# Kernel tuning notes

Measured on AMD Instinct MI355X. Metric: run time of the kernel, lower is better.

## Reference

```python
import jax, jax.numpy as jnp
import numpy as np

NUM_EXPERTS = 16
TOP_K = 2
D_IN = 1024
D_HID = 4096
D_OUT = 1024
BATCH = 8192


def setup_inputs() -> dict:
    key = jax.random.key(0)
    ks = jax.random.split(key, 6)
    s_in = 1.0 / np.sqrt(D_IN)
    s_hid = 1.0 / np.sqrt(D_HID)
    return {
        "x": jax.random.normal(ks[0], (BATCH, D_IN), dtype=jnp.float32),
        "Wg": jax.random.normal(ks[1], (D_IN, NUM_EXPERTS), dtype=jnp.float32) * s_in,
        "W1": jax.random.normal(ks[2], (NUM_EXPERTS, D_IN, D_HID), dtype=jnp.float32) * s_in,
        "b1": jnp.zeros((NUM_EXPERTS, D_HID), dtype=jnp.float32),
        "W2": jax.random.normal(ks[3], (NUM_EXPERTS, D_HID, D_OUT), dtype=jnp.float32) * s_hid,
        "b2": jnp.zeros((NUM_EXPERTS, D_OUT), dtype=jnp.float32),
    }


def _moe_forward(x, Wg, W1, b1, W2, b2):
    # Gating: top-k routing with softmax over the selected logits.
    logits = x @ Wg                                   # [B, E]
    top_vals, top_idx = jax.lax.top_k(logits, TOP_K)  # [B, k]
    routing_weights = jax.nn.softmax(top_vals, axis=-1)  # [B, k]

    # Per-token combine weight for each expert (sum over k slots):
    # cw[b, e] = sum_k routing_weights[b, k] * (top_idx[b, k] == e)
    one_hot = jax.nn.one_hot(top_idx, NUM_EXPERTS, dtype=x.dtype)  # [B, k, E]
    combine_w = jnp.einsum("bk,bke->be", routing_weights, one_hot)  # [B, E]

    # Per-expert MLP compute + weighted scatter-add combine.
    # Fixed-size loop over experts (structurally distinct weight slices);
    # equivalent math to the original's gather/compute/scatter dispatch.
    out = jnp.zeros((x.shape[0], D_OUT), dtype=x.dtype)
    for e in range(NUM_EXPERTS):
        h = jax.nn.relu(x @ W1[e] + b1[e])            # [B, H]
        y = h @ W2[e] + b2[e]                         # [B, O]
        out = out + combine_w[:, e:e + 1] * y
    return out


def reference(x, Wg, W1, b1, W2, b2):
    return _moe_forward(x, Wg, W1, b1, W2, b2)
```

## Files before the change

kernel.cpp:

```cpp
#include <hip/hip_runtime.h>
#include <cstdio>

#define DIN   1024
#define DHID  4096
#define DOUT  1024
#define NEXP  16
#define NTOK  8192
#define NPAIR (NTOK * 2)
#define PADMAX 18432
#define MAXTILES 144

typedef _Float16 h8 __attribute__((ext_vector_type(8)));
typedef _Float16 h4 __attribute__((ext_vector_type(4)));
typedef float    f4 __attribute__((ext_vector_type(4)));

#define C_CNT  0
#define C_POFF 16
#define C_CUR  32
#define C_NT   48
#define C_TE   64
#define C_TP   256

__device__ __forceinline__ void async16(const void* g, void* l) {
  __builtin_amdgcn_global_load_lds((const __attribute__((address_space(1))) void*)g,
                                   (__attribute__((address_space(3))) void*)l, 16, 0, 0);
}

__global__ void k_init(float* __restrict__ out, const float* __restrict__ x,
                       _Float16* __restrict__ x16, int* __restrict__ ptok,
                       float* __restrict__ pw, int* __restrict__ ctrl) {
  int i = blockIdx.x * 256 + threadIdx.x;
  ((f4*)out)[i] = (f4){0.f, 0.f, 0.f, 0.f};
  float4 v = ((const float4*)x)[i];
  h4 hv = {(_Float16)v.x, (_Float16)v.y, (_Float16)v.z, (_Float16)v.w};
  ((h4*)x16)[i] = hv;
  if (i < PADMAX) { ptok[i] = 0; pw[i] = 0.f; }
  if (i < 1024) ctrl[i] = 0;
}

__global__ void k_gate(const float* __restrict__ x, const float* __restrict__ wg,
                       int* __restrict__ te, float* __restrict__ tw,
                       int* __restrict__ ctrl) {
  int t = blockIdx.x * 4 + (threadIdx.x >> 6);
  int l = threadIdx.x & 63;
  const float* xr = x + (long)t * DIN;
  float acc[NEXP];
#pragma unroll
  for (int e = 0; e < NEXP; ++e) acc[e] = 0.f;
  for (int k = l; k < DIN; k += 64) {
    float xv = xr[k];
    const float4* wr = (const float4*)(wg + (long)k * NEXP);
    float4 a = wr[0], b = wr[1], c = wr[2], d = wr[3];
    acc[0]  += xv * a.x; acc[1]  += xv * a.y; acc[2]  += xv * a.z; acc[3]  += xv * a.w;
    acc[4]  += xv * b.x; acc[5]  += xv * b.y; acc[6]  += xv * b.z; acc[7]  += xv * b.w;
    acc[8]  += xv * c.x; acc[9]  += xv * c.y; acc[10] += xv * c.z; acc[11] += xv * c.w;
    acc[12] += xv * d.x; acc[13] += xv * d.y; acc[14] += xv * d.z; acc[15] += xv * d.w;
  }
#pragma unroll
  for (int off = 32; off > 0; off >>= 1) {
#pragma unroll
    for (int e = 0; e < NEXP; ++e) acc[e] += __shfl_xor(acc[e], off, 64);
  }
  if (l == 0) {
    float v0 = -1e30f; int e0 = 0;
#pragma unroll
    for (int e = 0; e < NEXP; ++e) if (acc[e] > v0) { v0 = acc[e]; e0 = e; }
    float v1 = -1e30f; int e1 = 0;
#pragma unroll
    for (int e = 0; e < NEXP; ++e) if (e != e0 && acc[e] > v1) { v1 = acc[e]; e1 = e; }
    float d = expf(v1 - v0);
    float den = 1.f / (1.f + d);
    te[2 * t] = e0;     tw[2 * t] = den;
    te[2 * t + 1] = e1; tw[2 * t + 1] = d * den;
    atomicAdd(&ctrl[C_CNT + e0], 1);
    atomicAdd(&ctrl[C_CNT + e1], 1);
  }
}

__global__ void k_scan(int* __restrict__ ctrl) {
  if (threadIdx.x != 0) return;
  int off = 0, nt = 0;
  for (int e = 0; e < NEXP; ++e) {
    int c = ctrl[C_CNT + e];
    int tiles = (c + 127) >> 7;
    ctrl[C_POFF + e] = off;
    ctrl[C_CUR + e] = off;
    for (int i = 0; i < tiles; ++i) { ctrl[C_TE + nt] = e; ctrl[C_TP + nt] = off + i * 128; ++nt; }
    off += tiles * 128;
  }
  ctrl[C_NT] = nt;
}

__global__ void k_assign(const int* __restrict__ te, const float* __restrict__ tw,
                         int* __restrict__ ctrl, int* __restrict__ ptok,
                         float* __restrict__ pw) {
  int t = blockIdx.x * 256 + threadIdx.x;
#pragma unroll
  for (int s = 0; s < 2; ++s) {
    int e = te[2 * t + s];
    int pos = atomicAdd(&ctrl[C_CUR + e], 1);
    ptok[pos] = t;
    pw[pos] = tw[2 * t + s];
  }
}

__global__ void k_transpose(const float* __restrict__ W, _Float16* __restrict__ out,
                            int R, int C) {
  __shared__ __align__(16) _Float16 tile[64][72];
  int e = blockIdx.z;
  const float* Wb = W + ((long)e * R + blockIdx.x * 64) * C + blockIdx.y * 64;
  int tid = threadIdx.x;
  int rr = tid >> 4;
  int cc = (tid & 15) * 4;
#pragma unroll
  for (int i = 0; i < 4; ++i) {
    int r = rr + i * 16;
    float4 v = *(const float4*)(Wb + (long)r * C + cc);
    tile[cc + 0][r] = (_Float16)v.x;
    tile[cc + 1][r] = (_Float16)v.y;
    tile[cc + 2][r] = (_Float16)v.z;
    tile[cc + 3][r] = (_Float16)v.w;
  }
  __syncthreads();
  _Float16* ob = out + ((long)e * C + blockIdx.y * 64) * R + blockIdx.x * 64;
  int c2 = tid >> 3;
  int ch = tid & 7;
#pragma unroll
  for (int i = 0; i < 2; ++i) {
    int c = c2 + i * 32;
    h8 v = *(const h8*)&tile[c][ch * 8];
    *(h8*)(ob + (long)c * R + ch * 8) = v;
  }
}

template<int KD, int ND, int G1>
__global__ __launch_bounds__(256)
void k_gemm(const _Float16* __restrict__ A, const _Float16* __restrict__ Wt,
            const float* __restrict__ bias, const int* __restrict__ ctrl,
            const int* __restrict__ ptok, const float* __restrict__ pw,
            _Float16* __restrict__ Hout, float* __restrict__ out) {
  __shared__ __align__(16) _Float16 As[128 * 64];
  __shared__ __align__(16) _Float16 Bs[128 * 64];
  int mt = blockIdx.y;
  if (mt >= ctrl[C_NT]) return;
  int e  = ctrl[C_TE + mt];
  int p0 = ctrl[C_TP + mt];
  int n0 = blockIdx.x * 128;
  int tid = threadIdx.x;
  int w = tid >> 6, l = tid & 63;
  int wm = w & 1, wn = w >> 1;
  int ln15 = l & 15, lq = l >> 4;

  const _Float16* ag[4];
  const _Float16* bg[4];
#pragma unroll
  for (int j = 0; j < 4; ++j) {
    int r = (w * 4 + j) * 8 + (l >> 3);
    int c = (l & 7) ^ (r & 7);
    long arow = G1 ? (long)ptok[p0 + r] : (long)(p0 + r);
    ag[j] = A + arow * KD + c * 8;
    bg[j] = Wt + ((long)e * ND + n0 + r) * KD + c * 8;
  }

  f4 acc[4][4];
#pragma unroll
  for (int i = 0; i < 4; ++i)
#pragma unroll
    for (int j = 0; j < 4; ++j) acc[i][j] = (f4){0.f, 0.f, 0.f, 0.f};

  for (int k0 = 0; k0 < KD; k0 += 64) {
#pragma unroll
    for (int j = 0; j < 4; ++j) {
      async16(ag[j] + k0, &As[(w * 4 + j) * 512]);
      async16(bg[j] + k0, &Bs[(w * 4 + j) * 512]);
    }
    __syncthreads();
#pragma unroll
    for (int ks = 0; ks < 2; ++ks) {
      h8 af[4], bf[4];
      int kq = ks * 4 + lq;
#pragma unroll
      for (int i = 0; i < 4; ++i) {
        int m = wm * 64 + i * 16 + ln15;
        af[i] = *(const h8*)&As[m * 64 + (kq ^ (m & 7)) * 8];
      }
#pragma unroll
      for (int j = 0; j < 4; ++j) {
        int n = wn * 64 + j * 16 + ln15;
        bf[j] = *(const h8*)&Bs[n * 64 + (kq ^ (n & 7)) * 8];
      }
#pragma unroll
      for (int i = 0; i < 4; ++i)
#pragma unroll
        for (int j = 0; j < 4; ++j)
          acc[i][j] = __builtin_amdgcn_mfma_f32_16x16x32_f16(af[i], bf[j], acc[i][j], 0, 0, 0);
    }
    __syncthreads();
  }

  float bj[4];
#pragma unroll
  for (int j = 0; j < 4; ++j) bj[j] = bias[e * ND + n0 + wn * 64 + j * 16 + ln15];

  if (G1) {
#pragma unroll
    for (int i = 0; i < 4; ++i)
#pragma unroll
      for (int reg = 0; reg < 4; ++reg) {
        int p = p0 + wm * 64 + i * 16 + lq * 4 + reg;
        _Float16* hr = Hout + (long)p * DHID + n0 + wn * 64 + ln15;
#pragma unroll
        for (int j = 0; j < 4; ++j)
          hr[j * 16] = (_Float16)fmaxf(acc[i][j][reg] + bj[j], 0.f);
      }
  } else {
#pragma unroll
    for (int i = 0; i < 4; ++i)
#pragma unroll
      for (int reg = 0; reg < 4; ++reg) {
        int p = p0 + wm * 64 + i * 16 + lq * 4 + reg;
        float wgt = pw[p];
        if (wgt != 0.f) {
          int t = ptok[p];
          float* orow = out + (long)t * DOUT + n0 + wn * 64 + ln15;
#pragma unroll
          for (int j = 0; j < 4; ++j)
            atomicAdd(&orow[j * 16], wgt * (acc[i][j][reg] + bj[j]));
        }
      }
  }
}

extern "C" void kernel_launch(void* const* d_in, const int* in_sizes, int n_in,
                              void* d_out, int out_size, void* d_ws, size_t ws_size,
                              hipStream_t stream) {
  const float* x  = (const float*)d_in[0];
  const float* Wg = (const float*)d_in[1];
  const float* W1 = (const float*)d_in[2];
  const float* b1 = (const float*)d_in[3];
  const float* W2 = (const float*)d_in[4];
  const float* b2 = (const float*)d_in[5];
  float* out = (float*)d_out;
  char* ws = (char*)d_ws;

  size_t WT_OFF = 0;
  size_t H_OFF  = WT_OFF + (size_t)NEXP * DHID * DIN * 2;
  size_t X_OFF  = H_OFF  + (size_t)PADMAX * DHID * 2;
  size_t TE_OFF = X_OFF  + (size_t)NTOK * DIN * 2;
  size_t TW_OFF = TE_OFF + (size_t)NPAIR * 4;
  size_t PT_OFF = TW_OFF + (size_t)NPAIR * 4;
  size_t PW_OFF = PT_OFF + (size_t)PADMAX * 4;
  size_t CT_OFF = PW_OFF + (size_t)PADMAX * 4;
  size_t END    = CT_OFF + 4096;
  if (ws_size < END) {
    fprintf(stderr, "kernel_launch: ws too small (%zu < %zu)\n", ws_size, END);
    return;
  }
  _Float16* Wt  = (_Float16*)(ws + WT_OFF);
  _Float16* H   = (_Float16*)(ws + H_OFF);
  _Float16* x16 = (_Float16*)(ws + X_OFF);
  int*   te   = (int*)(ws + TE_OFF);
  float* tw   = (float*)(ws + TW_OFF);
  int*   pt   = (int*)(ws + PT_OFF);
  float* pw   = (float*)(ws + PW_OFF);
  int*   ctrl = (int*)(ws + CT_OFF);

  k_init<<<NTOK * DIN / (256 * 4), 256, 0, stream>>>(out, x, x16, pt, pw, ctrl);
  k_gate<<<NTOK / 4, 256, 0, stream>>>(x, Wg, te, tw, ctrl);
  k_scan<<<1, 64, 0, stream>>>(ctrl);
  k_assign<<<NTOK / 256, 256, 0, stream>>>(te, tw, ctrl, pt, pw);

  k_transpose<<<dim3(DIN / 64, DHID / 64, NEXP), 256, 0, stream>>>(W1, Wt, DIN, DHID);
  k_gemm<DIN, DHID, 1><<<dim3(DHID / 128, MAXTILES), 256, 0, stream>>>(
      x16, Wt, b1, ctrl, pt, pw, H, nullptr);

  k_transpose<<<dim3(DHID / 64, DOUT / 64, NEXP), 256, 0, stream>>>(W2, Wt, DHID, DOUT);
  k_gemm<DHID, DOUT, 0><<<dim3(DOUT / 128, MAXTILES), 256, 0, stream>>>(
      H, Wt, b2, ctrl, pt, pw, nullptr, out);
}
```

Baseline: 1.365 ms.

## Use 256x256 MoE GEMM tiles with 8 waves, double-buffered LDS pipeline

```diff
diff --git a/kernel.cpp b/kernel.cpp
--- a/kernel.cpp
+++ b/kernel.cpp
@@ -7,8 +7,8 @@
 #define NEXP  16
 #define NTOK  8192
 #define NPAIR (NTOK * 2)
-#define PADMAX 18432
-#define MAXTILES 144
+#define PADMAX 20480
+#define MAXTILES 80
 
 typedef _Float16 h8 __attribute__((ext_vector_type(8)));
 typedef _Float16 h4 __attribute__((ext_vector_type(4)));
@@ -82,11 +82,11 @@
   int off = 0, nt = 0;
   for (int e = 0; e < NEXP; ++e) {
     int c = ctrl[C_CNT + e];
-    int tiles = (c + 127) >> 7;
+    int tiles = (c + 255) >> 8;
     ctrl[C_POFF + e] = off;
     ctrl[C_CUR + e] = off;
-    for (int i = 0; i < tiles; ++i) { ctrl[C_TE + nt] = e; ctrl[C_TP + nt] = off + i * 128; ++nt; }
-    off += tiles * 128;
+    for (int i = 0; i < tiles; ++i) { ctrl[C_TE + nt] = e; ctrl[C_TP + nt] = off + i * 256; ++nt; }
+    off += tiles * 256;
   }
   ctrl[C_NT] = nt;
 }
@@ -106,14 +106,14 @@
 
 __global__ void k_transpose(const float* __restrict__ W, _Float16* __restrict__ out,
                             int R, int C) {
-  __shared__ __align__(16) _Float16 tile[64][72];
+  __shared__ __align__(16) _Float16 tile[64][136];
   int e = blockIdx.z;
-  const float* Wb = W + ((long)e * R + blockIdx.x * 64) * C + blockIdx.y * 64;
+  const float* Wb = W + ((long)e * R + blockIdx.x * 128) * C + blockIdx.y * 64;
   int tid = threadIdx.x;
   int rr = tid >> 4;
   int cc = (tid & 15) * 4;
 #pragma unroll
-  for (int i = 0; i < 4; ++i) {
+  for (int i = 0; i < 8; ++i) {
     int r = rr + i * 16;
     float4 v = *(const float4*)(Wb + (long)r * C + cc);
     tile[cc + 0][r] = (_Float16)v.x;
@@ -122,112 +122,194 @@
     tile[cc + 3][r] = (_Float16)v.w;
   }
   __syncthreads();
-  _Float16* ob = out + ((long)e * C + blockIdx.y * 64) * R + blockIdx.x * 64;
-  int c2 = tid >> 3;
-  int ch = tid & 7;
-#pragma unroll
-  for (int i = 0; i < 2; ++i) {
-    int c = c2 + i * 32;
-    h8 v = *(const h8*)&tile[c][ch * 8];
-    *(h8*)(ob + (long)c * R + ch * 8) = v;
+  _Float16* ob = out + ((long)e * C + blockIdx.y * 64) * R + blockIdx.x * 128;
+  int c2 = tid >> 4;
+  int ch = tid & 15;
+#pragma unroll
+  for (int i = 0; i < 4; ++i) {
+    int c = c2 + i * 16;
+    *(h8*)(ob + (long)c * R + ch * 8) = *(const h8*)&tile[c][ch * 8];
   }
 }
 
 template<int KD, int ND, int G1>
-__global__ __launch_bounds__(256)
+__global__ __launch_bounds__(512, 2)
 void k_gemm(const _Float16* __restrict__ A, const _Float16* __restrict__ Wt,
             const float* __restrict__ bias, const int* __restrict__ ctrl,
             const int* __restrict__ ptok, const float* __restrict__ pw,
             _Float16* __restrict__ Hout, float* __restrict__ out) {
-  __shared__ __align__(16) _Float16 As[128 * 64];
-  __shared__ __align__(16) _Float16 Bs[128 * 64];
+  __shared__ __align__(16) _Float16 sm[65536];
+
   int mt = blockIdx.y;
   if (mt >= ctrl[C_NT]) return;
   int e  = ctrl[C_TE + mt];
   int p0 = ctrl[C_TP + mt];
-  int n0 = blockIdx.x * 128;
+  int n0 = blockIdx.x * 256;
   int tid = threadIdx.x;
   int w = tid >> 6, l = tid & 63;
   int wm = w & 1, wn = w >> 1;
   int ln15 = l & 15, lq = l >> 4;
 
-  const _Float16* ag[4];
-  const _Float16* bg[4];
-#pragma unroll
-  for (int j = 0; j < 4; ++j) {
-    int r = (w * 4 + j) * 8 + (l >> 3);
-    int c = (l & 7) ^ (r & 7);
-    long arow = G1 ? (long)ptok[p0 + r] : (long)(p0 + r);
-    ag[j] = A + arow * KD + c * 8;
-    bg[j] = Wt + ((long)e * ND + n0 + r) * KD + c * 8;
-  }
-
-  f4 acc[4][4];
-#pragma unroll
-  for (int i = 0; i < 4; ++i)
-#pragma unroll
-    for (int j = 0; j < 4; ++j) acc[i][j] = (f4){0.f, 0.f, 0.f, 0.f};
-
-  for (int k0 = 0; k0 < KD; k0 += 64) {
-#pragma unroll
-    for (int j = 0; j < 4; ++j) {
-      async16(ag[j] + k0, &As[(w * 4 + j) * 512]);
-      async16(bg[j] + k0, &Bs[(w * 4 + j) * 512]);
-    }
-    __syncthreads();
-#pragma unroll
-    for (int ks = 0; ks < 2; ++ks) {
-      h8 af[4], bf[4];
-      int kq = ks * 4 + lq;
-#pragma unroll
-      for (int i = 0; i < 4; ++i) {
-        int m = wm * 64 + i * 16 + ln15;
-        af[i] = *(const h8*)&As[m * 64 + (kq ^ (m & 7)) * 8];
+  const _Float16* agp[4];
+  const _Float16* bgp[4];
+#pragma unroll
+  for (int h = 0; h < 2; ++h)
+#pragma unroll
+    for (int j = 0; j < 2; ++j) {
+      int r = (w * 2 + j) * 8 + (l >> 3);
+      int c = (l & 7) ^ (r & 7);
+      long arow = G1 ? (long)ptok[p0 + h * 128 + r] : (long)(p0 + h * 128 + r);
+      agp[h * 2 + j] = A + arow * KD + c * 8;
+      bgp[h * 2 + j] = Wt + ((long)e * ND + n0 + h * 128 + r) * KD + c * 8;
+    }
+
+  auto stageH = [&](int t, int half) {
+    _Float16* dst = sm + (t & 1) * 32768 + (half & 1) * 16384 + (half >> 1) * 8192
+                    + w * 1024;
+    long koff = (long)t * 64;
+    const _Float16* const* gp = (half & 1) ? bgp : agp;
+#pragma unroll
+    for (int j = 0; j < 2; ++j)
+      async16(gp[(half >> 1) * 2 + j] + koff, dst + j * 512);
+  };
+
+  f4 acc[2][4][2][2];
+#pragma unroll
+  for (int mq = 0; mq < 2; ++mq)
+#pragma unroll
+    for (int i = 0; i < 4; ++i)
+#pragma unroll
+      for (int nq = 0; nq < 2; ++nq)
+#pragma unroll
+        for (int j = 0; j < 2; ++j) acc[mq][i][nq][j] = (f4){0.f, 0.f, 0.f, 0.f};
+
+  h8 af[8], bf0[4], bf1[4];
+
+  auto readA = [&](int d, int mq) {
+    const _Float16* Ab = sm + d * 32768 + mq * 8192;
+#pragma unroll
+    for (int i = 0; i < 4; ++i) {
+      int rh = wm * 64 + i * 16 + ln15;
+#pragma unroll
+      for (int ks = 0; ks < 2; ++ks)
+        af[i * 2 + ks] = *(const h8*)&Ab[rh * 64 + (((ks * 4 + lq)) ^ (rh & 7)) * 8];
+    }
+  };
+  auto readB = [&](int d, int nq, h8* bf) {
+    const _Float16* Bb = sm + d * 32768 + 16384 + nq * 8192;
+#pragma unroll
+    for (int j = 0; j < 2; ++j) {
+      int rh = wn * 32 + j * 16 + ln15;
+#pragma unroll
+      for (int ks = 0; ks < 2; ++ks)
+        bf[j * 2 + ks] = *(const h8*)&Bb[rh * 64 + (((ks * 4 + lq)) ^ (rh & 7)) * 8];
+    }
+  };
+  auto mfmaQ = [&](int mq, int nq, const h8* bf) {
+    __builtin_amdgcn_s_setprio(1);
+#pragma unroll
+    for (int ks = 0; ks < 2; ++ks)
+#pragma unroll
+      for (int i = 0; i < 4; ++i)
+#pragma unroll
+        for (int j = 0; j < 2; ++j)
+          acc[mq][i][nq][j] = __builtin_amdgcn_mfma_f32_16x16x32_f16(
+              af[i * 2 + ks], bf[j * 2 + ks], acc[mq][i][nq][j], 0, 0, 0);
+    __builtin_amdgcn_s_setprio(0);
+  };
+
+  constexpr int KSTEPS = KD / 64;
+
+  stageH(0, 0); stageH(0, 1); stageH(0, 2); stageH(0, 3);
+  stageH(1, 0); stageH(1, 1); stageH(1, 2);
+  asm volatile("s_waitcnt vmcnt(6)" ::: "memory");
+  __builtin_amdgcn_s_barrier();
+
+#pragma unroll 2
+  for (int t = 0; t < KSTEPS; ++t) {
+    int d = t & 1;
+    readA(d, 0);
+    readB(d, 0, bf0);
+    if (t + 1 < KSTEPS) stageH(t + 1, 3);
+    __builtin_amdgcn_s_barrier();
+    asm volatile("s_waitcnt lgkmcnt(0)" ::: "memory");
+    mfmaQ(0, 0, bf0);
+    __builtin_amdgcn_s_barrier();
+    readB(d, 1, bf1);
+    if (t + 2 < KSTEPS) stageH(t + 2, 0);
+    __builtin_amdgcn_s_barrier();
+    asm volatile("s_waitcnt lgkmcnt(0)" ::: "memory");
+    mfmaQ(0, 1, bf1);
+    __builtin_amdgcn_s_barrier();
+    readA(d, 1);
+    if (t + 2 < KSTEPS) stageH(t + 2, 1);
+    __builtin_amdgcn_s_barrier();
+    asm volatile("s_waitcnt lgkmcnt(0)" ::: "memory");
+    mfmaQ(1, 1, bf1);
+    __builtin_amdgcn_s_barrier();
+    if (t + 2 < KSTEPS) stageH(t + 2, 2);
+    if (t + 1 < KSTEPS) {
+      if (t + 2 < KSTEPS) asm volatile("s_waitcnt vmcnt(6)" ::: "memory");
+      else                asm volatile("s_waitcnt vmcnt(0)" ::: "memory");
+    }
+    __builtin_amdgcn_s_barrier();
+    mfmaQ(1, 0, bf0);
+    __builtin_amdgcn_s_barrier();
+  }
+
+  float bj[2][2];
+#pragma unroll
+  for (int nq = 0; nq < 2; ++nq)
+#pragma unroll
+    for (int j = 0; j < 2; ++j)
+      bj[nq][j] = bias[e * ND + n0 + nq * 128 + wn * 32 + j * 16 + ln15];
+
+  if (G1) {
+    _Float16* cs = sm;
+#pragma unroll
+    for (int mq = 0; mq < 2; ++mq) {
+      if (mq) __syncthreads();
+#pragma unroll
+      for (int i = 0; i < 4; ++i)
+#pragma unroll
+        for (int reg = 0; reg < 4; ++reg) {
+          int row = wm * 64 + i * 16 + lq * 4 + reg;
+#pragma unroll
+          for (int nq = 0; nq < 2; ++nq)
+#pragma unroll
+            for (int j = 0; j < 2; ++j)
+              cs[row * 264 + nq * 128 + wn * 32 + j * 16 + ln15] =
+                  (_Float16)fmaxf(acc[mq][i][nq][j][reg] + bj[nq][j], 0.f);
+        }
+      __syncthreads();
+#pragma unroll
+      for (int p = 0; p < 8; ++p) {
+        int idx = p * 512 + tid;
+        int row = idx >> 5, ch = idx & 31;
+        *(h8*)(Hout + (long)(p0 + mq * 128 + row) * DHID + n0 + ch * 8) =
+            *(const h8*)&cs[row * 264 + ch * 8];
       }
-#pragma unroll
-      for (int j = 0; j < 4; ++j) {
-        int n = wn * 64 + j * 16 + ln15;
-        bf[j] = *(const h8*)&Bs[n * 64 + (kq ^ (n & 7)) * 8];
-      }
+    }
+  } else {
+#pragma unroll
+    for (int mq = 0; mq < 2; ++mq)
 #pragma unroll
       for (int i = 0; i < 4; ++i)
 #pragma unroll
-        for (int j = 0; j < 4; ++j)
-          acc[i][j] = __builtin_amdgcn_mfma_f32_16x16x32_f16(af[i], bf[j], acc[i][j], 0, 0, 0);
-    }
-    __syncthreads();
-  }
-
-  float bj[4];
-#pragma unroll
-  for (int j = 0; j < 4; ++j) bj[j] = bias[e * ND + n0 + wn * 64 + j * 16 + ln15];
-
-  if (G1) {
-#pragma unroll
-    for (int i = 0; i < 4; ++i)
-#pragma unroll
-      for (int reg = 0; reg < 4; ++reg) {
-        int p = p0 + wm * 64 + i * 16 + lq * 4 + reg;
-        _Float16* hr = Hout + (long)p * DHID + n0 + wn * 64 + ln15;
-#pragma unroll
-        for (int j = 0; j < 4; ++j)
-          hr[j * 16] = (_Float16)fmaxf(acc[i][j][reg] + bj[j], 0.f);
-      }
-  } else {
-#pragma unroll
-    for (int i = 0; i < 4; ++i)
-#pragma unroll
-      for (int reg = 0; reg < 4; ++reg) {
-        int p = p0 + wm * 64 + i * 16 + lq * 4 + reg;
-        float wgt = pw[p];
-        if (wgt != 0.f) {
-          int t = ptok[p];
-          float* orow = out + (long)t * DOUT + n0 + wn * 64 + ln15;
-#pragma unroll
-          for (int j = 0; j < 4; ++j)
-            atomicAdd(&orow[j * 16], wgt * (acc[i][j][reg] + bj[j]));
+        for (int reg = 0; reg < 4; ++reg) {
+          int p = p0 + mq * 128 + wm * 64 + i * 16 + lq * 4 + reg;
+          float wgt = pw[p];
+          if (wgt != 0.f) {
+            int tk = ptok[p];
+            float* orow = out + (long)tk * DOUT + n0;
+#pragma unroll
+            for (int nq = 0; nq < 2; ++nq)
+#pragma unroll
+              for (int j = 0; j < 2; ++j)
+                atomicAdd(&orow[nq * 128 + wn * 32 + j * 16 + ln15],
+                          wgt * (acc[mq][i][nq][j][reg] + bj[nq][j]));
+          }
         }
-      }
   }
 }
 
@@ -270,11 +352,11 @@
   k_scan<<<1, 64, 0, stream>>>(ctrl);
   k_assign<<<NTOK / 256, 256, 0, stream>>>(te, tw, ctrl, pt, pw);
 
-  k_transpose<<<dim3(DIN / 64, DHID / 64, NEXP), 256, 0, stream>>>(W1, Wt, DIN, DHID);
-  k_gemm<DIN, DHID, 1><<<dim3(DHID / 128, MAXTILES), 256, 0, stream>>>(
+  k_transpose<<<dim3(DIN / 128, DHID / 64, NEXP), 256, 0, stream>>>(W1, Wt, DIN, DHID);
+  k_gemm<DIN, DHID, 1><<<dim3(DHID / 256, MAXTILES), 512, 0, stream>>>(
       x16, Wt, b1, ctrl, pt, pw, H, nullptr);
 
-  k_transpose<<<dim3(DHID / 64, DOUT / 64, NEXP), 256, 0, stream>>>(W2, Wt, DHID, DOUT);
-  k_gemm<DHID, DOUT, 0><<<dim3(DOUT / 128, MAXTILES), 256, 0, stream>>>(
+  k_transpose<<<dim3(DHID / 128, DOUT / 64, NEXP), 256, 0, stream>>>(W2, Wt, DHID, DOUT);
+  k_gemm<DHID, DOUT, 0><<<dim3(DOUT / 256, MAXTILES), 512, 0, stream>>>(
       H, Wt, b2, ctrl, pt, pw, nullptr, out);
 }
```

Result: faster. 1.289 ms (-5.6%).
